# Optimization experiments

Measured on AMD Instinct MI355X. Metric: run time of the kernel, lower is better.

The kernel has to match this reference:

```python
import jax, jax.numpy as jnp
import numpy as np

N_NODES = 50000
DIM = 128
NEG_SLOPE = 0.2


def _gat_conv(x, W, a_src, a_dst, b, src, dst, n):
    # PyG GATConv, single head, self-loops already appended to (src, dst).
    h = x @ W.T                              # [N, D]
    asrc = h @ a_src                         # [N]
    adst = h @ a_dst                         # [N]
    e = jax.nn.leaky_relu(asrc[src] + adst[dst], NEG_SLOPE)  # [E]
    emax = jax.ops.segment_max(e, dst, num_segments=n)
    emax = jnp.where(jnp.isfinite(emax), emax, 0.0)
    ex = jnp.exp(e - emax[dst])
    denom = jax.ops.segment_sum(ex, dst, num_segments=n)
    coef = ex / (denom[dst] + 1e-16)         # segment softmax over incoming edges
    out = jax.ops.segment_sum(coef[:, None] * h[src], dst, num_segments=n)
    return out + b


def _l2norm(x):
    # F.normalize(x) row-wise, eps=1e-12
    n = jnp.sqrt(jnp.sum(x * x, axis=1, keepdims=True))
    return x / jnp.maximum(n, 1e-12)


def setup_inputs() -> dict:
    key = jax.random.key(0)
    ks = jax.random.split(key, 24)
    d = DIM
    inp = {
        'entity_feat_1': jax.random.normal(ks[0], (N_NODES, d), jnp.float32),
        'image_feat': jax.random.normal(ks[1], (N_NODES, 4096), jnp.float32),
        'text_feat': jax.random.normal(ks[2], (N_NODES, 768), jnp.float32),
        'graph_edges': jax.random.randint(ks[3], (2, 600000), 0, N_NODES, jnp.int64),
        'entity_feat': jax.random.normal(ks[4], (N_NODES, d), jnp.float32) * (6.0 / (N_NODES + d)) ** 0.5 * 100,
        'W_img': jax.random.normal(ks[5], (d, 4096), jnp.float32) * 0.02,
        'b_img': jnp.zeros((d,), jnp.float32),
        'W_txt': jax.random.normal(ks[6], (d, 768), jnp.float32) * 0.03,
        'b_txt': jnp.zeros((d,), jnp.float32),
        'W_fus': jax.random.normal(ks[7], (d, 3 * d), jnp.float32) * 0.05,
        'b_fus': jnp.zeros((d,), jnp.float32),
    }
    for i, tag in enumerate(['e', 'i', 't']):
        base = 8 + 4 * i
        inp['W%s_gat' % tag] = jax.random.normal(ks[base], (d, d), jnp.float32) * 0.08
        inp['a%s_src' % tag] = jax.random.normal(ks[base + 1], (d,), jnp.float32) * 0.1
        inp['a%s_dst' % tag] = jax.random.normal(ks[base + 2], (d,), jnp.float32) * 0.1
        inp['b%s_gat' % tag] = jnp.zeros((d,), jnp.float32)
    return inp


def reference(entity_feat_1, image_feat, text_feat, graph_edges, entity_feat,
              W_img, b_img, W_txt, b_txt, W_fus, b_fus,
              We_gat, ae_src, ae_dst, be_gat,
              Wi_gat, ai_src, ai_dst, bi_gat,
              Wt_gat, at_src, at_dst, bt_gat):
    n = entity_feat.shape[0]
    loops = jnp.arange(n, dtype=graph_edges.dtype)
    src = jnp.concatenate([graph_edges[0], loops])
    dst = jnp.concatenate([graph_edges[1], loops])
    img = image_feat @ W_img.T + b_img
    txt = text_feat @ W_txt.T + b_txt
    # GraphConv = GATConv -> dropout(eval: identity) -> F.normalize
    e_out = _l2norm(_gat_conv(entity_feat, We_gat, ae_src, ae_dst, be_gat, src, dst, n))
    i_out = _l2norm(_gat_conv(img, Wi_gat, ai_src, ai_dst, bi_gat, src, dst, n))
    t_out = _l2norm(_gat_conv(txt, Wt_gat, at_src, at_dst, bt_gat, src, dst, n))
    mm = jnp.concatenate([e_out, i_out, t_out], axis=1) @ W_fus.T + b_fus
    return (e_out, i_out, t_out, mm)
```

## Files before the change

### kernel.cpp

```cpp
#include <hip/hip_runtime.h>
#include <hip/hip_bf16.h>

typedef __attribute__((ext_vector_type(8))) short bf16x8;
typedef __attribute__((ext_vector_type(4))) short bf16x4;
typedef __attribute__((ext_vector_type(4))) float f32x4;

#define LDS_A2 16384
#define LDS_HALF2 32768

__device__ __forceinline__ float fin(float v) {
    return (v == v && v > -1e30f && v < 1e30f) ? v : 0.f;
}
__device__ __forceinline__ float lrelu(float v) {
    return (v >= 0.f) ? v : 0.2f * v;
}
__device__ __forceinline__ unsigned f2bu(float f) {
    unsigned u = __builtin_bit_cast(unsigned, f);
    return (u + 0x7FFFu + ((u >> 16) & 1u)) >> 16;
}
__device__ __forceinline__ short f2b(float f) { return (short)f2bu(f); }
__device__ __forceinline__ float bflo(unsigned u) {
    return __builtin_bit_cast(float, u << 16);
}
__device__ __forceinline__ float bfhi(unsigned u) {
    return __builtin_bit_cast(float, u & 0xffff0000u);
}
__device__ __forceinline__ size_t swzidx(int r, int j, int K) {
    return (size_t)r * K + (j & ~63) + ((j & 63) ^ ((r & 7) << 3));
}

template<int FUSE, int AD, int HP, int NT, int AF16, int OSWZ>
__device__ __forceinline__
void gemm_body(const float* __restrict__ A0, const float* __restrict__ A1,
               const float* __restrict__ A2, const short* __restrict__ A16,
               const short* __restrict__ Bw,
               const float* __restrict__ bias,
               const float* __restrict__ av1, const float* __restrict__ av2,
               float* __restrict__ asrc, float* __restrict__ adst, int astride,
               float* __restrict__ Cf, short* __restrict__ C16s,
               unsigned* __restrict__ Cp, int cpstride,
               int M, int K, int bx)
{
    __shared__ __align__(16) char smem[2][LDS_HALF2];
    const int tid = threadIdx.x;
    const int l  = tid & 63;
    const int lr = l & 15;
    const int lk = l >> 4;
    const int w  = tid >> 6;
    const int brow = bx * 128;
    const int nt = K >> 6;

    f32x4 acc[8];
#pragma unroll
    for (int j = 0; j < 8; j++) acc[j] = (f32x4){0.f, 0.f, 0.f, 0.f};

    f32x4 va[4];

    auto stage_load = [&](int t, int buf) {
        if (AF16) {
#pragma unroll
            for (int i = 0; i < 2; i++) {
                int L   = (i * 512 + tid) * 16;
                int row = L >> 7;
                int Lr  = L & 127;
                int gr = brow + row; if (gr >= M) gr = M - 1;
                const short* gp = A16 + (size_t)gr * 128 + t * 64 + (Lr >> 1);
                __builtin_amdgcn_global_load_lds(
                    (const __attribute__((address_space(1))) void*)gp,
                    (__attribute__((address_space(3))) void*)&smem[buf][L],
                    16, 0, 0);
            }
        } else {
            const int k0 = t << 6;
#pragma unroll
            for (int i = 0; i < 4; i++) {
                int elem = (i * 512 + tid) * 4;
                int row = elem >> 6;
                int col = elem & 63;
                int gr = brow + row; if (gr >= M) gr = M - 1;
                int gcol = k0 + col;
                const float* p;
                if (FUSE) {
                    int seg = gcol >> 7;
                    const float* s = (seg == 0) ? A0 : (seg == 1) ? A1 : A2;
                    p = s + (size_t)gr * 128 + (gcol & 127);
                } else {
                    p = A0 + (size_t)gr * (size_t)K + gcol;
                }
                va[i] = NT ? __builtin_nontemporal_load((const f32x4*)p)
                           : *(const f32x4*)p;
            }
        }
#pragma unroll
        for (int i = 0; i < 2; i++) {
            int L   = (i * 512 + tid) * 16;
            int row = L >> 7;
            int Lr  = L & 127;
            const short* gp = Bw + (size_t)row * K + t * 64 + (Lr >> 1);
            __builtin_amdgcn_global_load_lds(
                (const __attribute__((address_space(1))) void*)gp,
                (__attribute__((address_space(3))) void*)&smem[buf][LDS_A2 + L],
                16, 0, 0);
        }
    };
    auto stage_write = [&](int buf) {
#pragma unroll
        for (int i = 0; i < 4; i++) {
            int elem = (i * 512 + tid) * 4;
            int row = elem >> 6;
            int col = elem & 63;
            int slo = (col * 2) ^ ((row & 7) << 4);
            bf16x4 a4 = {f2b(va[i].x), f2b(va[i].y), f2b(va[i].z), f2b(va[i].w)};
            *(bf16x4*)(&smem[buf][row * 128 + slo]) = a4;
        }
    };

    stage_load(0, 0);
    if (!AF16) stage_write(0);
    __syncthreads();
    int cur = 0;
    for (int t = 0; t < nt; t++) {
        if (t + 1 < nt) stage_load(t + 1, cur ^ 1);
        const char* Ab = &smem[cur][0];
        const char* Bb = &smem[cur][LDS_A2];
#pragma unroll
        for (int ks = 0; ks < 2; ks++) {
            bf16x8 af, bv[8];
            {
                int row = w * 16 + lr;
                int lo  = (ks * 64 + lk * 16) ^ ((row & 7) << 4);
                af = *(const bf16x8*)(Ab + row * 128 + lo);
            }
#pragma unroll
            for (int nf = 0; nf < 8; nf++) {
                int row = nf * 16 + lr;
                int lo  = (ks * 64 + lk * 16) ^ ((row & 7) << 4);
                bv[nf] = *(const bf16x8*)(Bb + row * 128 + lo);
            }
#pragma unroll
            for (int nf = 0; nf < 8; nf++)
                acc[nf] = __builtin_amdgcn_mfma_f32_16x16x32_bf16(
                    af, bv[nf], acc[nf], 0, 0, 0);
        }
        if (!AF16 && t + 1 < nt) stage_write(cur ^ 1);
        __syncthreads();
        cur ^= 1;
    }

#pragma unroll
    for (int j = 0; j < 4; j++) {
        int row = brow + w * 16 + lk * 4 + j;
        float vv[8];
        float s1 = 0.f, s2 = 0.f;
#pragma unroll
        for (int nf = 0; nf < 8; nf++) {
            int col = nf * 16 + lr;
            float v = acc[nf][j];
            if (bias) v += bias[col];
            v = fin(v);
            vv[nf] = v;
            if (AD) { s1 += v * av1[col]; s2 += v * av2[col]; }
            if (!HP && !OSWZ && row < M) Cf[(size_t)row * 128 + col] = v;
            if (OSWZ && row < M) C16s[swzidx(row, col, 128)] = f2b(v);
        }
        if (HP && row < M) {
#pragma unroll
            for (int nf = 0; nf < 4; nf++) {
                int col = nf * 16 + lr;
                Cp[(size_t)row * cpstride + col] = f2bu(vv[nf]) | (f2bu(vv[nf + 4]) << 16);
            }
        }
        if (AD) {
#pragma unroll
            for (int o = 1; o < 16; o <<= 1) {
                s1 += __shfl_xor(s1, o);
                s2 += __shfl_xor(s2, o);
            }
            if (lr == 0 && row < M) {
                asrc[(size_t)row * astride] = fin(s1);
                adst[(size_t)row * astride] = fin(s2);
            }
        }
    }
}

__global__ __launch_bounds__(512, 4)
void gemm_o16b(const float* __restrict__ x1, const float* __restrict__ x2,
               const short* __restrict__ w1, const short* __restrict__ w2,
               const float* __restrict__ b1, const float* __restrict__ b2,
               short* __restrict__ o1, short* __restrict__ o2,
               int M, int K1, int K2)
{
    int g = blockIdx.y;
    gemm_body<0, 0, 0, 1, 0, 1>(g ? x2 : x1, nullptr, nullptr, nullptr,
                                g ? w2 : w1, g ? b2 : b1,
                                nullptr, nullptr, nullptr, nullptr, 1,
                                nullptr, g ? o2 : o1, nullptr, 1,
                                M, g ? K2 : K1, blockIdx.x);
}

__global__ __launch_bounds__(512, 4)
void hgemm3b(const float* __restrict__ x0, const short* __restrict__ x1,
             const short* __restrict__ x2,
             const short* __restrict__ w0, const short* __restrict__ w1,
             const short* __restrict__ w2,
             const float* __restrict__ a10, const float* __restrict__ a11,
             const float* __restrict__ a12,
             const float* __restrict__ a20, const float* __restrict__ a21,
             const float* __restrict__ a22,
             unsigned* __restrict__ hpAll,
             float* __restrict__ asrc4, float* __restrict__ adst4, int M)
{
    int g = blockIdx.y;
    if (g == 0)
        gemm_body<0, 1, 1, 1, 0, 0>(x0, nullptr, nullptr, nullptr, w0, nullptr,
                                    a10, a20, asrc4 + 0, adst4 + 0, 4,
                                    nullptr, nullptr, hpAll + 0, 192,
                                    M, 128, blockIdx.x);
    else if (g == 1)
        gemm_body<0, 1, 1, 0, 1, 0>(nullptr, nullptr, nullptr, x1, w1, nullptr,
                                    a11, a21, asrc4 + 1, adst4 + 1, 4,
                                    nullptr, nullptr, hpAll + 64, 192,
                                    M, 128, blockIdx.x);
    else
        gemm_body<0, 1, 1, 0, 1, 0>(nullptr, nullptr, nullptr, x2, w2, nullptr,
                                    a12, a22, asrc4 + 2, adst4 + 2, 4,
                                    nullptr, nullptr, hpAll + 128, 192,
                                    M, 128, blockIdx.x);
}

__global__ __launch_bounds__(512, 4)
void gemm_fus(const float* __restrict__ A0, const float* __restrict__ A1,
              const float* __restrict__ A2, const short* __restrict__ Bw,
              const float* __restrict__ bias, float* __restrict__ Cf, int M)
{
    gemm_body<1, 0, 0, 0, 0, 0>(A0, A1, A2, nullptr, Bw, bias,
                                nullptr, nullptr, nullptr, nullptr, 1,
                                Cf, nullptr, nullptr, 1, M, 384, blockIdx.x);
}

__global__ void k_cvtN(const float* __restrict__ s0, const float* __restrict__ s1,
                       const float* __restrict__ s2, const float* __restrict__ s3,
                       short* __restrict__ d0, short* __restrict__ d1,
                       short* __restrict__ d2, short* __restrict__ d3,
                       int n0, int n1, int n2, int n3,
                       int K0, int K1, int K2, int K3)
{
    int g = blockIdx.y;
    const float* s = (g == 0) ? s0 : (g == 1) ? s1 : (g == 2) ? s2 : s3;
    short* d = (g == 0) ? d0 : (g == 1) ? d1 : (g == 2) ? d2 : d3;
    int n = (g == 0) ? n0 : (g == 1) ? n1 : (g == 2) ? n2 : n3;
    int K = (g == 0) ? K0 : (g == 1) ? K1 : (g == 2) ? K2 : K3;
    for (int i = blockIdx.x * blockDim.x + threadIdx.x; i * 4 < n;
         i += gridDim.x * blockDim.x) {
        int e = i * 4;
        int r = e / K;
        int j = e - r * K;
        f32x4 v = *(const f32x4*)(s + (size_t)e);
        bf16x4 b = {f2b(v.x), f2b(v.y), f2b(v.z), f2b(v.w)};
        *(bf16x4*)(d + swzidx(r, j, K)) = b;
    }
}

__global__ void k_init(const int* __restrict__ e, int* __restrict__ flag,
                       int* __restrict__ cnt, int n)
{
    if (blockIdx.x == 0 && threadIdx.x < 64) {
        int v = e[2 * threadIdx.x + 1];
        unsigned long long b = __ballot(v != 0);
        if (threadIdx.x == 0) flag[0] = (b == 0ull) ? 1 : 0;
    }
    for (int i = blockIdx.x * blockDim.x + threadIdx.x; i < n;
         i += gridDim.x * blockDim.x)
        cnt[i] = 0;
}

__global__ void k_scatter2(const int* __restrict__ e, const int* __restrict__ flag,
                           int* __restrict__ cnt, int* __restrict__ csr,
                           int e0, int n)
{
    int i = blockIdx.x * blockDim.x + threadIdx.x;
    if (i >= e0 + n) return;
    int s, d;
    if (i < e0) {
        if (flag[0]) { s = e[2 * i]; d = e[2 * e0 + 2 * i]; }
        else         { s = e[i];     d = e[e0 + i]; }
    } else {
        s = d = i - e0;
    }
    if ((unsigned)d >= (unsigned)n) d = 0;
    if ((unsigned)s >= (unsigned)n) s = 0;
    int pos = atomicAdd(&cnt[d], 1);
    if (pos < 64) csr[(size_t)d * 64 + pos] = s;
}

__global__ __launch_bounds__(256)
void gat3(const int* __restrict__ cnt, const int* __restrict__ csr,
          const unsigned* __restrict__ hpAll,
          const float* __restrict__ asrc4, const float* __restrict__ adst4,
          const float* __restrict__ bE, const float* __restrict__ bI,
          const float* __restrict__ bT,
          float* __restrict__ oE, float* __restrict__ oI, float* __restrict__ oT,
          int n)
{
    int node = blockIdx.x * 4 + (threadIdx.x >> 6);
    if (node >= n) return;
    int l = threadIdx.x & 63;
    int deg_n = cnt[node]; if (deg_n > 64) deg_n = 64;
    float adE = adst4[(size_t)node * 4 + 0];
    float adI = adst4[(size_t)node * 4 + 1];
    float adT = adst4[(size_t)node * 4 + 2];
    float aE0 = 0.f, aE1 = 0.f, aI0 = 0.f, aI1 = 0.f, aT0 = 0.f, aT1 = 0.f;

    bool valid = l < deg_n;
    int sidx = valid ? csr[(size_t)node * 64 + l] : 0;
    if ((unsigned)sidx >= (unsigned)n) sidx = 0;
    float eE = -1e30f, eI = -1e30f, eT = -1e30f;
    if (valid) {
        const float* ap = asrc4 + (size_t)sidx * 4;
        eE = lrelu(ap[0] + adE);
        eI = lrelu(ap[1] + adI);
        eT = lrelu(ap[2] + adT);
    }
    float mE = eE, mI = eI, mT = eT;
    for (int o = 32; o; o >>= 1) {
        mE = fmaxf(mE, __shfl_xor(mE, o));
        mI = fmaxf(mI, __shfl_xor(mI, o));
        mT = fmaxf(mT, __shfl_xor(mT, o));
    }
    float xE = valid ? __expf(eE - mE) : 0.f;
    float xI = valid ? __expf(eI - mI) : 0.f;
    float xT = valid ? __expf(eT - mT) : 0.f;
    float sE = xE, sI = xI, sT = xT;
    for (int o = 32; o; o >>= 1) {
        sE += __shfl_xor(sE, o);
        sI += __shfl_xor(sI, o);
        sT += __shfl_xor(sT, o);
    }
    float iE = 1.f / (sE + 1e-16f);
    float iI = 1.f / (sI + 1e-16f);
    float iT = 1.f / (sT + 1e-16f);
    for (int j = 0; j < deg_n; j++) {
        int   sj = __shfl(sidx, j);
        float cE = __shfl(xE, j) * iE;
        float cI = __shfl(xI, j) * iI;
        float cT = __shfl(xT, j) * iT;
        const unsigned* hb = hpAll + (size_t)sj * 192;
        unsigned uE = hb[l];
        unsigned uI = hb[64 + l];
        unsigned uT = hb[128 + l];
        aE0 += cE * bflo(uE); aE1 += cE * bfhi(uE);
        aI0 += cI * bflo(uI); aI1 += cI * bfhi(uI);
        aT0 += cT * bflo(uT); aT1 += cT * bfhi(uT);
    }

    {
        float a0 = aE0 + bE[l], a1 = aE1 + bE[64 + l];
        float ss = a0 * a0 + a1 * a1;
        for (int o = 32; o; o >>= 1) ss += __shfl_xor(ss, o);
        float r = 1.f / fmaxf(sqrtf(fin(ss)), 1e-12f);
        oE[(size_t)node * 128 + l]      = fin(a0 * r);
        oE[(size_t)node * 128 + 64 + l] = fin(a1 * r);
    }
    {
        float a0 = aI0 + bI[l], a1 = aI1 + bI[64 + l];
        float ss = a0 * a0 + a1 * a1;
        for (int o = 32; o; o >>= 1) ss += __shfl_xor(ss, o);
        float r = 1.f / fmaxf(sqrtf(fin(ss)), 1e-12f);
        oI[(size_t)node * 128 + l]      = fin(a0 * r);
        oI[(size_t)node * 128 + 64 + l] = fin(a1 * r);
    }
    {
        float a0 = aT0 + bT[l], a1 = aT1 + bT[64 + l];
        float ss = a0 * a0 + a1 * a1;
        for (int o = 32; o; o >>= 1) ss += __shfl_xor(ss, o);
        float r = 1.f / fmaxf(sqrtf(fin(ss)), 1e-12f);
        oT[(size_t)node * 128 + l]      = fin(a0 * r);
        oT[(size_t)node * 128 + 64 + l] = fin(a1 * r);
    }
}

extern "C" void kernel_launch(void* const* d_in, const int* in_sizes, int n_in,
                              void* d_out, int out_size, void* d_ws, size_t ws_size,
                              hipStream_t stream)
{
    int s0 = n_in - 22;
    if (s0 < 0 || s0 > 1)
        s0 = (in_sizes[1] > in_sizes[0]) ? 1 : 0;

    const float* image_feat  = (const float*)d_in[s0 + 0];
    const float* text_feat   = (const float*)d_in[s0 + 1];
    const int*   edges       = (const int*)d_in[s0 + 2];
    const float* entity_feat = (const float*)d_in[s0 + 3];
    const float* W_img = (const float*)d_in[s0 + 4];
    const float* b_img = (const float*)d_in[s0 + 5];
    const float* W_txt = (const float*)d_in[s0 + 6];
    const float* b_txt = (const float*)d_in[s0 + 7];
    const float* W_fus = (const float*)d_in[s0 + 8];
    const float* b_fus = (const float*)d_in[s0 + 9];
    const float* Wg[3]  = {(const float*)d_in[s0 + 10], (const float*)d_in[s0 + 14],
                           (const float*)d_in[s0 + 18]};
    const float* Avv[3] = {(const float*)d_in[s0 + 11], (const float*)d_in[s0 + 15],
                           (const float*)d_in[s0 + 19]};
    const float* Dvv[3] = {(const float*)d_in[s0 + 12], (const float*)d_in[s0 + 16],
                           (const float*)d_in[s0 + 20]};
    const float* Bg[3]  = {(const float*)d_in[s0 + 13], (const float*)d_in[s0 + 17],
                           (const float*)d_in[s0 + 21]};

    const int n  = in_sizes[s0 + 3] / 128;
    int e0 = in_sizes[s0 + 2] / 2;
    if (e0 == 24 * n) e0 = 12 * n;
    const int ne = e0 + n;
    const int Kimg = in_sizes[s0 + 4] / 128;
    const int Ktxt = in_sizes[s0 + 6] / 128;

    char* ws = (char*)d_ws;
    size_t off = 0;
    auto alloc = [&](size_t b) { size_t o = off; off = (off + b + 255) & ~(size_t)255; return o; };
    int* eflag  = (int*)(ws + alloc(256));
    int* cnt    = (int*)(ws + alloc((size_t)n * 4));
    int* csr    = (int*)(ws + alloc((size_t)n * 64 * 4));
    float* asrc4 = (float*)(ws + alloc((size_t)n * 16));
    float* adst4 = (float*)(ws + alloc((size_t)n * 16));
    short* Wimgb = (short*)(ws + alloc((size_t)Kimg * 128 * 2));
    short* Wtxtb = (short*)(ws + alloc((size_t)Ktxt * 128 * 2));
    short* Wgb0  = (short*)(ws + alloc(128 * 128 * 2));
    short* Wfusb = (short*)(ws + alloc(384 * 128 * 2));
    short* imgp16 = (short*)(ws + alloc((size_t)n * 128 * 2));
    short* txtp16 = (short*)(ws + alloc((size_t)n * 128 * 2));
    unsigned* hpAll = (unsigned*)(ws + alloc((size_t)n * 192 * 4));
    (void)ws_size; (void)out_size;

    float* out = (float*)d_out;
    float* oE = out;
    float* oI = out + (size_t)n * 128;
    float* oT = out + 2 * (size_t)n * 128;
    float* oM = out + 3 * (size_t)n * 128;

    k_init<<<208, 256, 0, stream>>>(edges, eflag, cnt, n);
    k_cvtN<<<dim3(128, 4), 256, 0, stream>>>(
        W_img, W_txt, Wg[0], W_fus,
        Wimgb, Wtxtb, Wgb0, Wfusb,
        Kimg * 128, Ktxt * 128, 128 * 128, 384 * 128,
        Kimg, Ktxt, 128, 384);
    k_scatter2<<<(ne + 255) / 256, 256, 0, stream>>>(edges, eflag, cnt, csr, e0, n);

    const int mb = (n + 127) / 128;
    gemm_o16b<<<dim3(mb, 2), 512, 0, stream>>>(image_feat, text_feat,
                                               Wimgb, Wtxtb, b_img, b_txt,
                                               imgp16, txtp16, n, Kimg, Ktxt);

    static_assert(true, "");
    short* Wgb1 = (short*)(ws + alloc(128 * 128 * 2));
    short* Wgb2 = (short*)(ws + alloc(128 * 128 * 2));
    k_cvtN<<<dim3(16, 2), 256, 0, stream>>>(
        Wg[1], Wg[2], Wg[1], Wg[2],
        Wgb1, Wgb2, Wgb1, Wgb2,
        128 * 128, 128 * 128, 0, 0,
        128, 128, 128, 128);

    hgemm3b<<<dim3(mb, 3), 512, 0, stream>>>(entity_feat, imgp16, txtp16,
                                             Wgb0, Wgb1, Wgb2,
                                             Avv[0], Avv[1], Avv[2],
                                             Dvv[0], Dvv[1], Dvv[2],
                                             hpAll, asrc4, adst4, n);

    gat3<<<(n + 3) / 4, 256, 0, stream>>>(cnt, csr, hpAll,
                                          asrc4, adst4, Bg[0], Bg[1], Bg[2],
                                          oE, oI, oT, n);

    gemm_fus<<<mb, 512, 0, stream>>>(oE, oI, oT, Wfusb, b_fus, oM, n);
}
```

Measured before the change: 393.2 us.

## Fuse modality projection with GAT linear layer in one two-stage GEMM kernel

The image/text projection GEMM and the following GAT weight GEMM are merged into a single kernel. The projected 128-wide tile stays in LDS as bf16, and a second MFMA pass multiplies it by the GAT weights. This removes the bf16 intermediate round trip through global memory and a launch. The weight conversions are also consolidated into one launch. In exchange, the entity-feature block (K=128) shares a grid with the long K=4096 image blocks, which can cause load imbalance across y-slices.

```diff
diff --git a/kernel.cpp b/kernel.cpp
--- a/kernel.cpp
+++ b/kernel.cpp
@@ -29,16 +29,16 @@
     return (size_t)r * K + (j & ~63) + ((j & 63) ^ ((r & 7) << 3));
 }
 
-template<int FUSE, int AD, int HP, int NT, int AF16, int OSWZ>
+template<int FUSE, int AD, int HP, int NT, int P2>
 __device__ __forceinline__
 void gemm_body(const float* __restrict__ A0, const float* __restrict__ A1,
-               const float* __restrict__ A2, const short* __restrict__ A16,
+               const float* __restrict__ A2,
                const short* __restrict__ Bw,
+               const short* __restrict__ W2,
                const float* __restrict__ bias,
                const float* __restrict__ av1, const float* __restrict__ av2,
                float* __restrict__ asrc, float* __restrict__ adst, int astride,
-               float* __restrict__ Cf, short* __restrict__ C16s,
-               unsigned* __restrict__ Cp, int cpstride,
+               float* __restrict__ Cf, unsigned* __restrict__ Cp, int cpstride,
                int M, int K, int bx)
 {
     __shared__ __align__(16) char smem[2][LDS_HALF2];
@@ -57,39 +57,24 @@
     f32x4 va[4];
 
     auto stage_load = [&](int t, int buf) {
-        if (AF16) {
-#pragma unroll
-            for (int i = 0; i < 2; i++) {
-                int L   = (i * 512 + tid) * 16;
-                int row = L >> 7;
-                int Lr  = L & 127;
-                int gr = brow + row; if (gr >= M) gr = M - 1;
-                const short* gp = A16 + (size_t)gr * 128 + t * 64 + (Lr >> 1);
-                __builtin_amdgcn_global_load_lds(
-                    (const __attribute__((address_space(1))) void*)gp,
-                    (__attribute__((address_space(3))) void*)&smem[buf][L],
-                    16, 0, 0);
-            }
-        } else {
-            const int k0 = t << 6;
-#pragma unroll
-            for (int i = 0; i < 4; i++) {
-                int elem = (i * 512 + tid) * 4;
-                int row = elem >> 6;
-                int col = elem & 63;
-                int gr = brow + row; if (gr >= M) gr = M - 1;
-                int gcol = k0 + col;
-                const float* p;
-                if (FUSE) {
-                    int seg = gcol >> 7;
-                    const float* s = (seg == 0) ? A0 : (seg == 1) ? A1 : A2;
-                    p = s + (size_t)gr * 128 + (gcol & 127);
-                } else {
-                    p = A0 + (size_t)gr * (size_t)K + gcol;
-                }
-                va[i] = NT ? __builtin_nontemporal_load((const f32x4*)p)
-                           : *(const f32x4*)p;
-            }
+        const int k0 = t << 6;
+#pragma unroll
+        for (int i = 0; i < 4; i++) {
+            int elem = (i * 512 + tid) * 4;
+            int row = elem >> 6;
+            int col = elem & 63;
+            int gr = brow + row; if (gr >= M) gr = M - 1;
+            int gcol = k0 + col;
+            const float* p;
+            if (FUSE) {
+                int seg = gcol >> 7;
+                const float* s = (seg == 0) ? A0 : (seg == 1) ? A1 : A2;
+                p = s + (size_t)gr * 128 + (gcol & 127);
+            } else {
+                p = A0 + (size_t)gr * (size_t)K + gcol;
+            }
+            va[i] = NT ? __builtin_nontemporal_load((const f32x4*)p)
+                       : *(const f32x4*)p;
         }
 #pragma unroll
         for (int i = 0; i < 2; i++) {
@@ -116,7 +101,7 @@
     };
 
     stage_load(0, 0);
-    if (!AF16) stage_write(0);
+    stage_write(0);
     __syncthreads();
     int cur = 0;
     for (int t = 0; t < nt; t++) {
@@ -142,9 +127,70 @@
                 acc[nf] = __builtin_amdgcn_mfma_f32_16x16x32_bf16(
                     af, bv[nf], acc[nf], 0, 0, 0);
         }
-        if (!AF16 && t + 1 < nt) stage_write(cur ^ 1);
+        if (t + 1 < nt) stage_write(cur ^ 1);
         __syncthreads();
         cur ^= 1;
+    }
+
+    if (P2) {
+        char* Cb = &smem[0][0];
+        char* Wb = &smem[1][0];
+#pragma unroll
+        for (int i = 0; i < 4; i++) {
+            int L = (i * 512 + tid) * 16;
+            int half = L >> 14;
+            int Lh = L & 16383;
+            int row = Lh >> 7;
+            int Lr = Lh & 127;
+            const short* gp = W2 + (size_t)row * 128 + half * 64 + (Lr >> 1);
+            __builtin_amdgcn_global_load_lds(
+                (const __attribute__((address_space(1))) void*)gp,
+                (__attribute__((address_space(3))) void*)&Wb[L],
+                16, 0, 0);
+        }
+#pragma unroll
+        for (int j = 0; j < 4; j++) {
+            int row = w * 16 + lk * 4 + j;
+#pragma unroll
+            for (int nf = 0; nf < 8; nf++) {
+                int col = nf * 16 + lr;
+                float v = acc[nf][j];
+                if (bias) v += bias[col];
+                v = fin(v);
+                int half = col >> 6;
+                int ch = col & 63;
+                *(short*)(&Cb[half * 16384 + row * 128 +
+                              ((ch * 2) ^ ((row & 7) << 4))]) = f2b(v);
+            }
+        }
+        __syncthreads();
+        f32x4 acc2[8];
+#pragma unroll
+        for (int j = 0; j < 8; j++) acc2[j] = (f32x4){0.f, 0.f, 0.f, 0.f};
+#pragma unroll
+        for (int t2 = 0; t2 < 2; t2++) {
+#pragma unroll
+            for (int ks = 0; ks < 2; ks++) {
+                bf16x8 af, bv[8];
+                {
+                    int row = w * 16 + lr;
+                    int lo  = (ks * 64 + lk * 16) ^ ((row & 7) << 4);
+                    af = *(const bf16x8*)(Cb + t2 * 16384 + row * 128 + lo);
+                }
+#pragma unroll
+                for (int nf = 0; nf < 8; nf++) {
+                    int row = nf * 16 + lr;
+                    int lo  = (ks * 64 + lk * 16) ^ ((row & 7) << 4);
+                    bv[nf] = *(const bf16x8*)(Wb + t2 * 16384 + row * 128 + lo);
+                }
+#pragma unroll
+                for (int nf = 0; nf < 8; nf++)
+                    acc2[nf] = __builtin_amdgcn_mfma_f32_16x16x32_bf16(
+                        af, bv[nf], acc2[nf], 0, 0, 0);
+            }
+        }
+#pragma unroll
+        for (int j = 0; j < 8; j++) acc[j] = acc2[j];
     }
 
 #pragma unroll
@@ -156,12 +202,11 @@
         for (int nf = 0; nf < 8; nf++) {
             int col = nf * 16 + lr;
             float v = acc[nf][j];
-            if (bias) v += bias[col];
+            if (!P2 && bias) v += bias[col];
             v = fin(v);
             vv[nf] = v;
             if (AD) { s1 += v * av1[col]; s2 += v * av2[col]; }
-            if (!HP && !OSWZ && row < M) Cf[(size_t)row * 128 + col] = v;
-            if (OSWZ && row < M) C16s[swzidx(row, col, 128)] = f2b(v);
+            if (!HP && row < M) Cf[(size_t)row * 128 + col] = v;
         }
         if (HP && row < M) {
 #pragma unroll
@@ -185,48 +230,33 @@
 }
 
 __global__ __launch_bounds__(512, 4)
-void gemm_o16b(const float* __restrict__ x1, const float* __restrict__ x2,
-               const short* __restrict__ w1, const short* __restrict__ w2,
-               const float* __restrict__ b1, const float* __restrict__ b2,
-               short* __restrict__ o1, short* __restrict__ o2,
-               int M, int K1, int K2)
-{
-    int g = blockIdx.y;
-    gemm_body<0, 0, 0, 1, 0, 1>(g ? x2 : x1, nullptr, nullptr, nullptr,
-                                g ? w2 : w1, g ? b2 : b1,
-                                nullptr, nullptr, nullptr, nullptr, 1,
-                                nullptr, g ? o2 : o1, nullptr, 1,
-                                M, g ? K2 : K1, blockIdx.x);
-}
-
-__global__ __launch_bounds__(512, 4)
-void hgemm3b(const float* __restrict__ x0, const short* __restrict__ x1,
-             const short* __restrict__ x2,
-             const short* __restrict__ w0, const short* __restrict__ w1,
-             const short* __restrict__ w2,
-             const float* __restrict__ a10, const float* __restrict__ a11,
-             const float* __restrict__ a12,
-             const float* __restrict__ a20, const float* __restrict__ a21,
-             const float* __restrict__ a22,
-             unsigned* __restrict__ hpAll,
-             float* __restrict__ asrc4, float* __restrict__ adst4, int M)
+void projh3(const float* __restrict__ xe, const float* __restrict__ xi,
+            const float* __restrict__ xt,
+            const short* __restrict__ w0, const short* __restrict__ wi,
+            const short* __restrict__ wt,
+            const short* __restrict__ wg1, const short* __restrict__ wg2,
+            const float* __restrict__ bi, const float* __restrict__ bt,
+            const float* __restrict__ a10, const float* __restrict__ a11,
+            const float* __restrict__ a12,
+            const float* __restrict__ a20, const float* __restrict__ a21,
+            const float* __restrict__ a22,
+            unsigned* __restrict__ hpAll,
+            float* __restrict__ asrc4, float* __restrict__ adst4,
+            int M, int Kimg, int Ktxt)
 {
     int g = blockIdx.y;
     if (g == 0)
-        gemm_body<0, 1, 1, 1, 0, 0>(x0, nullptr, nullptr, nullptr, w0, nullptr,
-                                    a10, a20, asrc4 + 0, adst4 + 0, 4,
-                                    nullptr, nullptr, hpAll + 0, 192,
-                                    M, 128, blockIdx.x);
+        gemm_body<0, 1, 1, 1, 0>(xe, nullptr, nullptr, w0, nullptr, nullptr,
+                                 a10, a20, asrc4 + 0, adst4 + 0, 4,
+                                 nullptr, hpAll + 0, 192, M, 128, blockIdx.x);
     else if (g == 1)
-        gemm_body<0, 1, 1, 0, 1, 0>(nullptr, nullptr, nullptr, x1, w1, nullptr,
-                                    a11, a21, asrc4 + 1, adst4 + 1, 4,
-                                    nullptr, nullptr, hpAll + 64, 192,
-                                    M, 128, blockIdx.x);
+        gemm_body<0, 1, 1, 1, 1>(xi, nullptr, nullptr, wi, wg1, bi,
+                                 a11, a21, asrc4 + 1, adst4 + 1, 4,
+                                 nullptr, hpAll + 64, 192, M, Kimg, blockIdx.x);
     else
-        gemm_body<0, 1, 1, 0, 1, 0>(nullptr, nullptr, nullptr, x2, w2, nullptr,
-                                    a12, a22, asrc4 + 2, adst4 + 2, 4,
-                                    nullptr, nullptr, hpAll + 128, 192,
-                                    M, 128, blockIdx.x);
+        gemm_body<0, 1, 1, 1, 1>(xt, nullptr, nullptr, wt, wg2, bt,
+                                 a12, a22, asrc4 + 2, adst4 + 2, 4,
+                                 nullptr, hpAll + 128, 192, M, Ktxt, blockIdx.x);
 }
 
 __global__ __launch_bounds__(512, 4)
@@ -234,23 +264,29 @@
               const float* __restrict__ A2, const short* __restrict__ Bw,
               const float* __restrict__ bias, float* __restrict__ Cf, int M)
 {
-    gemm_body<1, 0, 0, 0, 0, 0>(A0, A1, A2, nullptr, Bw, bias,
-                                nullptr, nullptr, nullptr, nullptr, 1,
-                                Cf, nullptr, nullptr, 1, M, 384, blockIdx.x);
+    gemm_body<1, 0, 0, 0, 0>(A0, A1, A2, Bw, nullptr, bias,
+                             nullptr, nullptr, nullptr, nullptr, 1,
+                             Cf, nullptr, 1, M, 384, blockIdx.x);
 }
 
 __global__ void k_cvtN(const float* __restrict__ s0, const float* __restrict__ s1,
                        const float* __restrict__ s2, const float* __restrict__ s3,
+                       const float* __restrict__ s4, const float* __restrict__ s5,
                        short* __restrict__ d0, short* __restrict__ d1,
                        short* __restrict__ d2, short* __restrict__ d3,
-                       int n0, int n1, int n2, int n3,
-                       int K0, int K1, int K2, int K3)
+                       short* __restrict__ d4, short* __restrict__ d5,
+                       int n0, int n1, int n2, int n3, int n4, int n5,
+                       int K0, int K1, int K2, int K3, int K4, int K5)
 {
     int g = blockIdx.y;
-    const float* s = (g == 0) ? s0 : (g == 1) ? s1 : (g == 2) ? s2 : s3;
-    short* d = (g == 0) ? d0 : (g == 1) ? d1 : (g == 2) ? d2 : d3;
-    int n = (g == 0) ? n0 : (g == 1) ? n1 : (g == 2) ? n2 : n3;
-    int K = (g == 0) ? K0 : (g == 1) ? K1 : (g == 2) ? K2 : K3;
+    const float* s = (g == 0) ? s0 : (g == 1) ? s1 : (g == 2) ? s2
+                   : (g == 3) ? s3 : (g == 4) ? s4 : s5;
+    short* d = (g == 0) ? d0 : (g == 1) ? d1 : (g == 2) ? d2
+             : (g == 3) ? d3 : (g == 4) ? d4 : d5;
+    int n = (g == 0) ? n0 : (g == 1) ? n1 : (g == 2) ? n2
+          : (g == 3) ? n3 : (g == 4) ? n4 : n5;
+    int K = (g == 0) ? K0 : (g == 1) ? K1 : (g == 2) ? K2
+          : (g == 3) ? K3 : (g == 4) ? K4 : K5;
     for (int i = blockIdx.x * blockDim.x + threadIdx.x; i * 4 < n;
          i += gridDim.x * blockDim.x) {
         int e = i * 4;
@@ -425,9 +461,9 @@
     short* Wimgb = (short*)(ws + alloc((size_t)Kimg * 128 * 2));
     short* Wtxtb = (short*)(ws + alloc((size_t)Ktxt * 128 * 2));
     short* Wgb0  = (short*)(ws + alloc(128 * 128 * 2));
+    short* Wgb1  = (short*)(ws + alloc(128 * 128 * 2));
+    short* Wgb2  = (short*)(ws + alloc(128 * 128 * 2));
     short* Wfusb = (short*)(ws + alloc(384 * 128 * 2));
-    short* imgp16 = (short*)(ws + alloc((size_t)n * 128 * 2));
-    short* txtp16 = (short*)(ws + alloc((size_t)n * 128 * 2));
     unsigned* hpAll = (unsigned*)(ws + alloc((size_t)n * 192 * 4));
     (void)ws_size; (void)out_size;
 
@@ -438,32 +474,21 @@
     float* oM = out + 3 * (size_t)n * 128;
 
     k_init<<<208, 256, 0, stream>>>(edges, eflag, cnt, n);
-    k_cvtN<<<dim3(128, 4), 256, 0, stream>>>(
-        W_img, W_txt, Wg[0], W_fus,
-        Wimgb, Wtxtb, Wgb0, Wfusb,
-        Kimg * 128, Ktxt * 128, 128 * 128, 384 * 128,
-        Kimg, Ktxt, 128, 384);
+    k_cvtN<<<dim3(128, 6), 256, 0, stream>>>(
+        W_img, W_txt, Wg[0], Wg[1], Wg[2], W_fus,
+        Wimgb, Wtxtb, Wgb0, Wgb1, Wgb2, Wfusb,
+        Kimg * 128, Ktxt * 128, 128 * 128, 128 * 128, 128 * 128, 384 * 128,
+        Kimg, Ktxt, 128, 128, 128, 384);
     k_scatter2<<<(ne + 255) / 256, 256, 0, stream>>>(edges, eflag, cnt, csr, e0, n);
 
     const int mb = (n + 127) / 128;
-    gemm_o16b<<<dim3(mb, 2), 512, 0, stream>>>(image_feat, text_feat,
-                                               Wimgb, Wtxtb, b_img, b_txt,
-                                               imgp16, txtp16, n, Kimg, Ktxt);
-
-    static_assert(true, "");
-    short* Wgb1 = (short*)(ws + alloc(128 * 128 * 2));
-    short* Wgb2 = (short*)(ws + alloc(128 * 128 * 2));
-    k_cvtN<<<dim3(16, 2), 256, 0, stream>>>(
-        Wg[1], Wg[2], Wg[1], Wg[2],
-        Wgb1, Wgb2, Wgb1, Wgb2,
-        128 * 128, 128 * 128, 0, 0,
-        128, 128, 128, 128);
-
-    hgemm3b<<<dim3(mb, 3), 512, 0, stream>>>(entity_feat, imgp16, txtp16,
-                                             Wgb0, Wgb1, Wgb2,
-                                             Avv[0], Avv[1], Avv[2],
-                                             Dvv[0], Dvv[1], Dvv[2],
-                                             hpAll, asrc4, adst4, n);
+    projh3<<<dim3(mb, 3), 512, 0, stream>>>(entity_feat, image_feat, text_feat,
+                                            Wgb0, Wimgb, Wtxtb, Wgb1, Wgb2,
+                                            b_img, b_txt,
+                                            Avv[0], Avv[1], Avv[2],
+                                            Dvv[0], Dvv[1], Dvv[2],
+                                            hpAll, asrc4, adst4,
+                                            n, Kimg, Ktxt);
 
     gat3<<<(n + 3) / 4, 256, 0, stream>>>(cnt, csr, hpAll,
                                           asrc4, adst4, Bg[0], Bg[1], Bg[2],
```

Result: slower. 438.1 us (+11.4%).
